# Optimization experiments

Measured on AMD Instinct MI355X. Metric: run time of the kernel, lower is better.

## Reference

```python
import jax, jax.numpy as jnp
import numpy as np

TAU = 0.05


def setup_inputs() -> dict:
    key = jax.random.key(0)
    ks = jax.random.split(key, 4)
    N, D, F, E = 8192, 1024, 4096, 8
    h = jax.random.normal(ks[0], (N, D), dtype=jnp.float32)
    Wr = jax.random.normal(ks[1], (D, E), dtype=jnp.float32) * (1.0 / np.sqrt(D))
    br = jnp.zeros((E,), dtype=jnp.float32)
    W1 = jax.random.normal(ks[2], (E, D, F), dtype=jnp.float32) * (1.0 / np.sqrt(D))
    b1 = jnp.zeros((E, F), dtype=jnp.float32)
    W2 = jax.random.normal(ks[3], (E, F, D), dtype=jnp.float32) * (1.0 / np.sqrt(F))
    b2 = jnp.zeros((E, D), dtype=jnp.float32)
    return {"h": h, "Wr": Wr, "br": br, "W1": W1, "b1": b1, "W2": W2, "b2": b2}


def reference(h, Wr, br, W1, b1, W2, b2):
    # Router: linear + softmax over experts -> [N, E]
    weights = jax.nn.softmax(h @ Wr + br, axis=-1)
    # Threshold mask (weights > tau); masked_weights = weights * mask
    masked_w = jnp.where(weights > TAU, weights, 0.0)  # [N, E]
    # Experts: 2-layer MLP per expert, computed batched over the expert axis.
    # hid: [N, E, F]
    hid = jax.nn.gelu(jnp.einsum('nd,edf->nef', h, W1) + b1)
    # expert outputs: [N, E, D]
    out_e = jnp.einsum('nef,efd->ned', hid, W2) + b2
    # Weighted combine; zero masked weights annihilate inactive experts,
    # matching the conditional sum (and the zeros_like fallback when none active).
    return jnp.einsum('ne,ned->nd', masked_w, out_e)
```

## Files before the change

### kernel.cpp

```cpp
#include <hip/hip_runtime.h>
#include <hip/hip_bf16.h>
#include <cstdint>
#include <cstddef>

typedef __attribute__((ext_vector_type(8))) __bf16 bf16x8;
typedef __attribute__((ext_vector_type(4))) float f32x4;
typedef __attribute__((ext_vector_type(4))) unsigned short us4;

#define GLOAD_LDS16(g, l)                                                        \
    __builtin_amdgcn_global_load_lds(                                            \
        (const __attribute__((address_space(1))) void*)(g),                      \
        (__attribute__((address_space(3))) void*)(l), 16, 0, 0)

static __device__ __forceinline__ unsigned short f2bf(float x) {
    unsigned int u = __builtin_bit_cast(unsigned int, x);
    return (unsigned short)((u + 0x7FFFu + ((u >> 16) & 1u)) >> 16);
}

static __device__ __forceinline__ float gelu_fast(float x) {
    const float p = x * x;
    const float u = x * fmaf(0.0713548162726f, p, 1.59576912161f);
    const float t = __expf(-u);
    return x * __builtin_amdgcn_rcpf(1.0f + t);
}

__global__ __launch_bounds__(256) void moe_router_kernel(
    const float* __restrict__ h, const float* __restrict__ Wr,
    const float* __restrict__ br, unsigned short* __restrict__ hbf,
    float* __restrict__ mw)
{
    const int lane = threadIdx.x & 63, wave = threadIdx.x >> 6;
    const int n = blockIdx.x * 4 + wave;
    const float* hr = h + (size_t)n * 1024;
    const int base = lane * 16;

    float xs[16];
#pragma unroll
    for (int q = 0; q < 4; ++q) {
        f32x4 v = *(const f32x4*)(hr + base + q * 4);
        xs[q * 4 + 0] = v[0]; xs[q * 4 + 1] = v[1];
        xs[q * 4 + 2] = v[2]; xs[q * 4 + 3] = v[3];
    }
    float acc[8] = {0.f, 0.f, 0.f, 0.f, 0.f, 0.f, 0.f, 0.f};
#pragma unroll
    for (int j = 0; j < 16; ++j) {
        const float x = xs[j];
        const f32x4 w0 = *(const f32x4*)(Wr + (size_t)(base + j) * 8);
        const f32x4 w1 = *(const f32x4*)(Wr + (size_t)(base + j) * 8 + 4);
        acc[0] += x * w0[0]; acc[1] += x * w0[1]; acc[2] += x * w0[2]; acc[3] += x * w0[3];
        acc[4] += x * w1[0]; acc[5] += x * w1[1]; acc[6] += x * w1[2]; acc[7] += x * w1[3];
    }
#pragma unroll
    for (int q = 0; q < 4; ++q) {
        us4 o;
        o[0] = f2bf(xs[q * 4 + 0]); o[1] = f2bf(xs[q * 4 + 1]);
        o[2] = f2bf(xs[q * 4 + 2]); o[3] = f2bf(xs[q * 4 + 3]);
        *(us4*)(hbf + (size_t)n * 1024 + base + q * 4) = o;
    }
#pragma unroll
    for (int m = 32; m >= 1; m >>= 1)
#pragma unroll
        for (int e = 0; e < 8; ++e) acc[e] += __shfl_xor(acc[e], m, 64);

    if (lane == 0) {
        float l[8]; float mx = -1e30f;
#pragma unroll
        for (int e = 0; e < 8; ++e) { l[e] = acc[e] + br[e]; mx = fmaxf(mx, l[e]); }
        float s = 0.f;
#pragma unroll
        for (int e = 0; e < 8; ++e) { l[e] = __expf(l[e] - mx); s += l[e]; }
        const float inv = 1.0f / s;
#pragma unroll
        for (int e = 0; e < 8; ++e) {
            const float w = l[e] * inv;
            mw[(size_t)n * 8 + e] = (w > 0.05f) ? w : 0.0f;
        }
    }
}

__global__ __launch_bounds__(256) void moe_tcvt_kernel(
    const float* __restrict__ in, unsigned short* __restrict__ out,
    int ls, size_t in_es, int os, size_t out_es)
{
    __shared__ unsigned short t[32][33];
    const int e = blockIdx.z;
    const int r = threadIdx.x >> 3, c = (threadIdx.x & 7) * 4;
    const float* I = in + (size_t)e * in_es + (size_t)(blockIdx.x * 32 + r) * ls + blockIdx.y * 32 + c;
    f32x4 v = *(const f32x4*)I;
    t[r][c + 0] = f2bf(v[0]); t[r][c + 1] = f2bf(v[1]);
    t[r][c + 2] = f2bf(v[2]); t[r][c + 3] = f2bf(v[3]);
    __syncthreads();
    unsigned short* O = out + (size_t)e * out_es + (size_t)(blockIdx.y * 32 + r) * os + blockIdx.x * 32 + c;
    us4 o;
    o[0] = t[c + 0][r]; o[1] = t[c + 1][r]; o[2] = t[c + 2][r]; o[3] = t[c + 3][r];
    *(us4*)O = o;
}

#define MFMA_QUAD(MB, NB, AF, BQ)                                              \
  _Pragma("unroll") for (int mi_ = 0; mi_ < 4; ++mi_)                          \
  _Pragma("unroll") for (int ni_ = 0; ni_ < 2; ++ni_) {                        \
      acc[(MB)+mi_][(NB)+ni_] = __builtin_amdgcn_mfma_f32_16x16x32_bf16(       \
          BQ[ni_][1], AF[mi_][1], __builtin_amdgcn_mfma_f32_16x16x32_bf16(     \
          BQ[ni_][0], AF[mi_][0], acc[(MB)+mi_][(NB)+ni_], 0, 0, 0), 0, 0, 0); \
  }

#define BARX()   __builtin_amdgcn_s_barrier()
#define SBX()    __builtin_amdgcn_sched_barrier(0)
#define LGKM(N)  asm volatile("s_waitcnt lgkmcnt(" #N ")" ::: "memory")
#define VMC(N)   asm volatile("s_waitcnt vmcnt(" #N ")" ::: "memory")
#define PRIO1()  __builtin_amdgcn_s_setprio(1)
#define PRIO0()  __builtin_amdgcn_s_setprio(0)

template <int MODE>
__global__ __launch_bounds__(512) void moe_gemm8p(
    const unsigned short* __restrict__ A, int ldga,
    const unsigned short* __restrict__ Bbase, size_t estride, int ldb,
    const float* __restrict__ b1, const float* __restrict__ mw,
    unsigned short* __restrict__ Cg, int ldc,
    float* __restrict__ part,
    int logFc, int f0glob, int kspan, int init)
{
    __shared__ unsigned short sh[65536];
    char* sm = (char*)sh;
    const int XA = 0, XB = 32768, YA = 65536, YB = 98304;

    const int tid = threadIdx.x, lane = tid & 63, wv = tid >> 6;
    const int wr = wv >> 2, wc = wv & 3;

    int bx, by;
    if constexpr (MODE == 0) {
        const int orig = blockIdx.x + blockIdx.y * 32;
        const int c8 = orig & 7, j = orig >> 3;
        bx = c8 * 4 + (j & 3); by = j >> 2;
    } else {
        const int orig = blockIdx.x + blockIdx.y * 32;
        const int c8 = orig & 7, j = orig >> 3;
        bx = c8 * 4 + (j >> 2); by = j & 3;
    }
    const int m0 = bx * 256;
    const int n0 = by * 256;

    const int z = (MODE == 1) ? blockIdx.z : 0;
    const int klo = z * kspan;
    float* Cacc = (MODE == 1) ? part + (size_t)z * (8192 * 1024) : nullptr;

    int e0 = 0, fb = 0;
    const unsigned short* gB0 = nullptr;
    const int rl0 = tid >> 3;
    const int gs8 = ((tid & 7) ^ (rl0 & 7)) * 8;
    if constexpr (MODE == 0) {
        e0 = n0 >> logFc; fb = n0 - (e0 << logFc);
        gB0 = Bbase + (size_t)e0 * estride + (size_t)(fb + rl0) * ldb + gs8;
    }
    const unsigned short* gA0 = A + (size_t)(m0 + rl0) * ldga + gs8;
    const int dstw = wv * 1024;

    auto stageA = [&](int reg, int kk, int q) {
        GLOAD_LDS16(gA0 + kk + (size_t)(q * 64) * ldga,
                    sm + reg + (q >> 1) * 16384 + (q & 1) * 8192 + dstw);
    };
    auto stageB = [&](int reg, int kk, int q) {
        const unsigned short* gb;
        if constexpr (MODE == 0) {
            gb = gB0 + kk;
        } else {
            const int e = kk >> logFc, kc = kk - (e << logFc);
            gb = Bbase + (size_t)e * estride + (size_t)(n0 + rl0) * ldb + kc + gs8;
        }
        GLOAD_LDS16(gb + (size_t)(q * 64) * ldb,
                    sm + reg + (q >> 1) * 16384 + (q & 1) * 8192 + dstw);
    };

    const int l15 = lane & 15, l4 = lane >> 4, l7 = lane & 7;
    const int sA0 = (wr * 128 + l15) * 128 + (((0 + l4) ^ l7) << 4);
    const int sA1 = (wr * 128 + l15) * 128 + (((4 + l4) ^ l7) << 4);
    const int sB0 = (wc * 64 + l15) * 128 + (((0 + l4) ^ l7) << 4);
    const int sB1 = (wc * 64 + l15) * 128 + (((4 + l4) ^ l7) << 4);

    f32x4 acc[8][4] = {};
    bf16x8 afL[4][2], afH[4][2], bqL[2][2], bqH[2][2];

#define RD_AFL(BASE) _Pragma("unroll") for (int mi_=0;mi_<4;++mi_){            \
      afL[mi_][0] = *(const bf16x8*)(sm + (BASE) + sA0 + mi_*2048);            \
      afL[mi_][1] = *(const bf16x8*)(sm + (BASE) + sA1 + mi_*2048); }
#define RD_AFH(BASE) _Pragma("unroll") for (int mi_=0;mi_<4;++mi_){            \
      afH[mi_][0] = *(const bf16x8*)(sm + (BASE) + sA0 + (4+mi_)*2048);        \
      afH[mi_][1] = *(const bf16x8*)(sm + (BASE) + sA1 + (4+mi_)*2048); }
#define RD_BQL(BASE) _Pragma("unroll") for (int ni_=0;ni_<2;++ni_){            \
      bqL[ni_][0] = *(const bf16x8*)(sm + (BASE) + sB0 + ni_*2048);            \
      bqL[ni_][1] = *(const bf16x8*)(sm + (BASE) + sB1 + ni_*2048); }
#define RD_BQH(BASE) _Pragma("unroll") for (int ni_=0;ni_<2;++ni_){            \
      bqH[ni_][0] = *(const bf16x8*)(sm + (BASE) + sB0 + (2+ni_)*2048);        \
      bqH[ni_][1] = *(const bf16x8*)(sm + (BASE) + sB1 + (2+ni_)*2048); }

    const int niter = kspan >> 7;

#pragma unroll
    for (int q = 0; q < 4; ++q) { stageA(XA, klo, q); stageB(XB, klo, q); }
#pragma unroll
    for (int q = 0; q < 4; ++q) { stageA(YA, klo + 64, q); stageB(YB, klo + 64, q); }
    VMC(8); SBX();
    BARX();
    RD_AFL(XA); RD_BQL(XB);

    for (int it = 0; it < niter; ++it) {
        const int kX2 = klo + it * 128 + 128;
        const int kY2 = klo + it * 128 + 192;
        const bool g = (it + 1 < niter);
        RD_BQH(XB);
        BARX(); LGKM(4); SBX(); PRIO1(); MFMA_QUAD(0, 0, afL, bqL); PRIO0(); BARX();
        RD_AFH(XA);
        if (g) { stageA(XA, kX2, 0); stageA(XA, kX2, 2); }
        BARX(); LGKM(8); SBX(); PRIO1(); MFMA_QUAD(0, 2, afL, bqH); PRIO0(); BARX();
        if (g) { stageB(XB, kX2, 0); stageB(XB, kX2, 1); }
        BARX(); LGKM(0); SBX(); PRIO1(); MFMA_QUAD(4, 0, afH, bqL); PRIO0(); BARX();
        if (g) { stageA(XA, kX2, 1); stageA(XA, kX2, 3);
                 stageB(XB, kX2, 2); stageB(XB, kX2, 3);
                 VMC(8); } else { VMC(0); }
        SBX();
        BARX();
        RD_AFL(YA); RD_BQL(YB);
        SBX(); PRIO1(); MFMA_QUAD(4, 2, afH, bqH); PRIO0(); BARX();
        RD_BQH(YB);
        BARX(); LGKM(4); SBX(); PRIO1(); MFMA_QUAD(0, 0, afL, bqL); PRIO0(); BARX();
        RD_AFH(YA);
        if (g) { stageA(YA, kY2, 0); stageA(YA, kY2, 2); }
        BARX(); LGKM(8); SBX(); PRIO1(); MFMA_QUAD(0, 2, afL, bqH); PRIO0(); BARX();
        if (g) { stageB(YB, kY2, 0); stageB(YB, kY2, 1); }
        BARX(); LGKM(0); SBX(); PRIO1(); MFMA_QUAD(4, 0, afH, bqL); PRIO0(); BARX();
        if (g) { stageA(YA, kY2, 1); stageA(YA, kY2, 3);
                 stageB(YB, kY2, 2); stageB(YB, kY2, 3);
                 VMC(8); } else { VMC(0); }
        SBX();
        BARX();
        if (g) { RD_AFL(XA); RD_BQL(XB); }
        SBX(); PRIO1(); MFMA_QUAD(4, 2, afH, bqH); PRIO0(); BARX();
    }

    const int nr0v = l4 * 4;
    if constexpr (MODE == 0) {
        const float* b1p = b1 + (size_t)e0 * 4096 + f0glob + fb;
        f32x4 b1v[4];
#pragma unroll
        for (int j = 0; j < 4; ++j)
            b1v[j] = *(const f32x4*)(b1p + wc * 64 + j * 16 + nr0v);
#pragma unroll
        for (int i = 0; i < 8; ++i) {
            const int token = m0 + wr * 128 + i * 16 + l15;
            const float w = mw[(size_t)token * 8 + e0];
            unsigned short* crow = Cg + (size_t)token * ldc + n0;
#pragma unroll
            for (int j = 0; j < 4; ++j) {
                const int n = wc * 64 + j * 16 + nr0v;
                us4 o;
#pragma unroll
                for (int r = 0; r < 4; ++r)
                    o[r] = f2bf(w * gelu_fast(acc[i][j][r] + b1v[j][r]));
                *(us4*)(crow + n) = o;
            }
        }
    } else {
#pragma unroll
        for (int i = 0; i < 8; ++i) {
            const int row = m0 + wr * 128 + i * 16 + l15;
            float* cp = Cacc + (size_t)row * 1024 + n0;
#pragma unroll
            for (int j = 0; j < 4; ++j) {
                const int n = wc * 64 + j * 16 + nr0v;
                if (init) {
                    *(f32x4*)(cp + n) = acc[i][j];
                } else {
                    f32x4 old = *(const f32x4*)(cp + n);
                    *(f32x4*)(cp + n) = old + acc[i][j];
                }
            }
        }
    }
}

__global__ __launch_bounds__(256) void moe_combine_kernel(
    const float* __restrict__ part, int S,
    float* __restrict__ out, const float* __restrict__ mw,
    const float* __restrict__ b2)
{
    const int n = blockIdx.x, t = threadIdx.x;
    const int d = t * 4;
    f32x4 v = *(const f32x4*)(part + (size_t)n * 1024 + d);
    for (int z = 1; z < S; ++z)
        v = v + *(const f32x4*)(part + (size_t)z * (8192 * 1024) + (size_t)n * 1024 + d);
#pragma unroll
    for (int e = 0; e < 8; ++e) {
        const float w = mw[(size_t)n * 8 + e];
        const f32x4 b = *(const f32x4*)(b2 + (size_t)e * 1024 + d);
        v = v + w * b;
    }
    *(f32x4*)(out + (size_t)n * 1024 + d) = v;
}

extern "C" void kernel_launch(void* const* d_in, const int* in_sizes, int n_in,
                              void* d_out, int out_size, void* d_ws, size_t ws_size,
                              hipStream_t stream)
{
    (void)in_sizes; (void)n_in; (void)out_size;
    const float* h  = (const float*)d_in[0];
    const float* Wr = (const float*)d_in[1];
    const float* br = (const float*)d_in[2];
    const float* W1 = (const float*)d_in[3];
    const float* b1 = (const float*)d_in[4];
    const float* W2 = (const float*)d_in[5];
    const float* b2 = (const float*)d_in[6];
    float* out = (float*)d_out;

    const int N = 8192, D = 1024, F = 4096, E = 8;
    const int S = 2;
    auto al = [](size_t x) { return (x + 255) & ~(size_t)255; };
    const size_t sz_hbf = al((size_t)N * D * 2);
    const size_t sz_mw  = al((size_t)N * E * 4);
    const size_t sz_pt1 = al((size_t)N * D * 4);
    auto tot = [&](int fc) {
        size_t s = sz_hbf + sz_mw + al((size_t)N * ((size_t)E * fc + 32) * 2);
        s += al((size_t)E * fc * D * 2) * 2;
        s += (size_t)S * sz_pt1;
        return s;
    };
    int Fc;
    if      (tot(1024) <= ws_size) Fc = 1024;
    else if (tot(512)  <= ws_size) Fc = 512;
    else                           Fc = 256;
    const int logFc = (Fc == 1024) ? 10 : (Fc == 512) ? 9 : 8;
    const int Kc = E * Fc;
    const int ldAp = Kc + 32;

    char* p = (char*)d_ws;
    unsigned short* hbf = (unsigned short*)p; p += sz_hbf;
    float* mwp  = (float*)p; p += sz_mw;
    unsigned short* ghid = (unsigned short*)p; p += al((size_t)N * (size_t)ldAp * 2);
    unsigned short* W1t  = (unsigned short*)p; p += al((size_t)E * Fc * D * 2);
    unsigned short* W2t  = (unsigned short*)p; p += al((size_t)E * Fc * D * 2);
    float* part = (float*)p;

    moe_router_kernel<<<N / 4, 256, 0, stream>>>(h, Wr, br, hbf, mwp);

    const int nch = F / Fc;
    for (int c = 0; c < nch; ++c) {
        moe_tcvt_kernel<<<dim3(D / 32, Fc / 32, E), 256, 0, stream>>>(
            W1 + (size_t)c * Fc, W1t, F, (size_t)D * F, D, (size_t)Fc * D);
        moe_tcvt_kernel<<<dim3(Fc / 32, D / 32, E), 256, 0, stream>>>(
            W2 + (size_t)c * Fc * D, W2t, D, (size_t)F * D, Fc, (size_t)D * Fc);

        moe_gemm8p<0><<<dim3(32, Kc / 256, 1), 512, 0, stream>>>(
            hbf, 1024, W1t, (size_t)Fc * D, 1024, b1, mwp, ghid, ldAp, nullptr,
            logFc, c * Fc, 1024, 0);

        moe_gemm8p<1><<<dim3(32, 4, S), 512, 0, stream>>>(
            ghid, ldAp, W2t, (size_t)D * Fc, Fc, nullptr, nullptr, nullptr, 0, part,
            logFc, 0, Kc / S, (c == 0) ? 1 : 0);
    }

    moe_combine_kernel<<<N, 256, 0, stream>>>(part, S, out, mwp, b2);
}
```

Baseline: 1.243 ms.

## Gather active tokens per expert to skip inactive rows in first GEMM

Adds a compaction kernel that builds a per-expert list of tokens whose routing weight passes the threshold, and makes the first expert GEMM gather A rows through that list and exit early for tiles past the active count. Inactive (token, expert) hidden slices are zero-filled once up front so the second GEMM stays dense and still correct. It also raises the preferred F chunk size so fewer chunk iterations are launched. The cost is extra kernels, a memset and an atomic, gathered global loads for A, and a larger workspace requirement.

```diff
diff --git a/kernel.cpp b/kernel.cpp
--- a/kernel.cpp
+++ b/kernel.cpp
@@ -74,6 +74,48 @@
         for (int e = 0; e < 8; ++e) {
             const float w = l[e] * inv;
             mw[(size_t)n * 8 + e] = (w > 0.05f) ? w : 0.0f;
+        }
+    }
+}
+
+__global__ __launch_bounds__(256) void moe_compact_kernel(
+    const float* __restrict__ mw, int* __restrict__ cnt, int* __restrict__ toklist)
+{
+    const int n = blockIdx.x * 256 + threadIdx.x;
+    const int lane = threadIdx.x & 63;
+#pragma unroll
+    for (int e = 0; e < 8; ++e) {
+        const bool act = mw[(size_t)n * 8 + e] > 0.f;
+        const unsigned long long mask = __ballot(act);
+        const int cw = __popcll(mask);
+        if (cw) {
+            int base = 0;
+            const int leader = __ffsll((unsigned long long)mask) - 1;
+            if (lane == leader) base = atomicAdd(&cnt[e], cw);
+            base = __shfl(base, leader);
+            if (act) {
+                const int pre = __popcll(mask & ((1ull << lane) - 1ull));
+                toklist[e * 8192 + base + pre] = n;
+            }
+        }
+    }
+}
+
+__global__ __launch_bounds__(256) void moe_zfill_kernel(
+    const float* __restrict__ mw, unsigned short* __restrict__ ghid,
+    int Fc, int ldAp)
+{
+    const int n = blockIdx.x, t = threadIdx.x;
+    __shared__ float w[8];
+    if (t < 8) w[t] = mw[(size_t)n * 8 + t];
+    __syncthreads();
+    const us4 z = {0, 0, 0, 0};
+#pragma unroll
+    for (int e = 0; e < 8; ++e) {
+        if (w[e] == 0.f) {
+            unsigned short* row = ghid + (size_t)n * ldAp + e * Fc;
+            for (int c = t * 4; c < Fc; c += 1024)
+                *(us4*)(row + c) = z;
         }
     }
 }
@@ -118,6 +160,7 @@
     const float* __restrict__ b1, const float* __restrict__ mw,
     unsigned short* __restrict__ Cg, int ldc,
     float* __restrict__ part,
+    const int* __restrict__ cnt, const int* __restrict__ toklist,
     int logFc, int f0glob, int kspan, int init)
 {
     __shared__ unsigned short sh[65536];
@@ -148,16 +191,39 @@
     const unsigned short* gB0 = nullptr;
     const int rl0 = tid >> 3;
     const int gs8 = ((tid & 7) ^ (rl0 & 7)) * 8;
+    const int l15 = lane & 15, l4 = lane >> 4, l7 = lane & 7;
+
+    int Me = 0;
+    int idxS[4], idxE[8];
     if constexpr (MODE == 0) {
         e0 = n0 >> logFc; fb = n0 - (e0 << logFc);
         gB0 = Bbase + (size_t)e0 * estride + (size_t)(fb + rl0) * ldb + gs8;
+        Me = cnt[e0];
+        if (m0 >= Me) return;
+        const int* tl = toklist + e0 * 8192;
+#pragma unroll
+        for (int q = 0; q < 4; ++q) {
+            int pos = m0 + rl0 + q * 64; if (pos > Me - 1) pos = Me - 1;
+            idxS[q] = tl[pos];
+        }
+#pragma unroll
+        for (int i = 0; i < 8; ++i) {
+            int pos = m0 + wr * 128 + i * 16 + l15; if (pos > Me - 1) pos = Me - 1;
+            idxE[i] = tl[pos];
+        }
+        VMC(0); SBX();
     }
     const unsigned short* gA0 = A + (size_t)(m0 + rl0) * ldga + gs8;
     const int dstw = wv * 1024;
 
     auto stageA = [&](int reg, int kk, int q) {
-        GLOAD_LDS16(gA0 + kk + (size_t)(q * 64) * ldga,
-                    sm + reg + (q >> 1) * 16384 + (q & 1) * 8192 + dstw);
+        const unsigned short* ga;
+        if constexpr (MODE == 0) {
+            ga = A + (size_t)idxS[q] * ldga + gs8 + kk;
+        } else {
+            ga = gA0 + kk + (size_t)(q * 64) * ldga;
+        }
+        GLOAD_LDS16(ga, sm + reg + (q >> 1) * 16384 + (q & 1) * 8192 + dstw);
     };
     auto stageB = [&](int reg, int kk, int q) {
         const unsigned short* gb;
@@ -171,7 +237,6 @@
                     sm + reg + (q >> 1) * 16384 + (q & 1) * 8192 + dstw);
     };
 
-    const int l15 = lane & 15, l4 = lane >> 4, l7 = lane & 7;
     const int sA0 = (wr * 128 + l15) * 128 + (((0 + l4) ^ l7) << 4);
     const int sA1 = (wr * 128 + l15) * 128 + (((4 + l4) ^ l7) << 4);
     const int sB0 = (wc * 64 + l15) * 128 + (((0 + l4) ^ l7) << 4);
@@ -246,17 +311,20 @@
             b1v[j] = *(const f32x4*)(b1p + wc * 64 + j * 16 + nr0v);
 #pragma unroll
         for (int i = 0; i < 8; ++i) {
-            const int token = m0 + wr * 128 + i * 16 + l15;
-            const float w = mw[(size_t)token * 8 + e0];
-            unsigned short* crow = Cg + (size_t)token * ldc + n0;
-#pragma unroll
-            for (int j = 0; j < 4; ++j) {
-                const int n = wc * 64 + j * 16 + nr0v;
-                us4 o;
-#pragma unroll
-                for (int r = 0; r < 4; ++r)
-                    o[r] = f2bf(w * gelu_fast(acc[i][j][r] + b1v[j][r]));
-                *(us4*)(crow + n) = o;
+            const int pos = m0 + wr * 128 + i * 16 + l15;
+            if (pos < Me) {
+                const int token = idxE[i];
+                const float w = mw[(size_t)token * 8 + e0];
+                unsigned short* crow = Cg + (size_t)token * ldc + n0;
+#pragma unroll
+                for (int j = 0; j < 4; ++j) {
+                    const int n = wc * 64 + j * 16 + nr0v;
+                    us4 o;
+#pragma unroll
+                    for (int r = 0; r < 4; ++r)
+                        o[r] = f2bf(w * gelu_fast(acc[i][j][r] + b1v[j][r]));
+                    *(us4*)(crow + n) = o;
+                }
             }
         }
     } else {
@@ -316,30 +384,38 @@
     auto al = [](size_t x) { return (x + 255) & ~(size_t)255; };
     const size_t sz_hbf = al((size_t)N * D * 2);
     const size_t sz_mw  = al((size_t)N * E * 4);
+    const size_t sz_cnt = al(8 * 4);
+    const size_t sz_tok = al((size_t)N * E * 4);
     const size_t sz_pt1 = al((size_t)N * D * 4);
     auto tot = [&](int fc) {
-        size_t s = sz_hbf + sz_mw + al((size_t)N * ((size_t)E * fc + 32) * 2);
-        s += al((size_t)E * fc * D * 2) * 2;
-        s += (size_t)S * sz_pt1;
+        size_t s = sz_hbf + sz_mw + sz_cnt + sz_tok
+                 + al((size_t)N * ((size_t)E * fc + 32) * 2)
+                 + al((size_t)E * fc * D * 2) * 2
+                 + (size_t)S * sz_pt1;
         return s;
     };
     int Fc;
-    if      (tot(1024) <= ws_size) Fc = 1024;
-    else if (tot(512)  <= ws_size) Fc = 512;
-    else                           Fc = 256;
-    const int logFc = (Fc == 1024) ? 10 : (Fc == 512) ? 9 : 8;
+    if      (tot(2048) <= ws_size) Fc = 2048;
+    else if (tot(1024) <= ws_size) Fc = 1024;
+    else                           Fc = 512;
+    const int logFc = (Fc == 2048) ? 11 : (Fc == 1024) ? 10 : 9;
     const int Kc = E * Fc;
     const int ldAp = Kc + 32;
 
     char* p = (char*)d_ws;
     unsigned short* hbf = (unsigned short*)p; p += sz_hbf;
     float* mwp  = (float*)p; p += sz_mw;
+    int*   cnt  = (int*)p;   p += sz_cnt;
+    int*   tok  = (int*)p;   p += sz_tok;
     unsigned short* ghid = (unsigned short*)p; p += al((size_t)N * (size_t)ldAp * 2);
     unsigned short* W1t  = (unsigned short*)p; p += al((size_t)E * Fc * D * 2);
     unsigned short* W2t  = (unsigned short*)p; p += al((size_t)E * Fc * D * 2);
     float* part = (float*)p;
 
     moe_router_kernel<<<N / 4, 256, 0, stream>>>(h, Wr, br, hbf, mwp);
+    hipMemsetAsync(cnt, 0, 8 * sizeof(int), stream);
+    moe_compact_kernel<<<N / 256, 256, 0, stream>>>(mwp, cnt, tok);
+    moe_zfill_kernel<<<N, 256, 0, stream>>>(mwp, ghid, Fc, ldAp);
 
     const int nch = F / Fc;
     for (int c = 0; c < nch; ++c) {
@@ -350,11 +426,11 @@
 
         moe_gemm8p<0><<<dim3(32, Kc / 256, 1), 512, 0, stream>>>(
             hbf, 1024, W1t, (size_t)Fc * D, 1024, b1, mwp, ghid, ldAp, nullptr,
-            logFc, c * Fc, 1024, 0);
+            cnt, tok, logFc, c * Fc, 1024, 0);
 
         moe_gemm8p<1><<<dim3(32, 4, S), 512, 0, stream>>>(
             ghid, ldAp, W2t, (size_t)D * Fc, Fc, nullptr, nullptr, nullptr, 0, part,
-            logFc, 0, Kc / S, (c == 0) ? 1 : 0);
+            nullptr, nullptr, logFc, 0, Kc / S, (c == 0) ? 1 : 0);
     }
 
     moe_combine_kernel<<<N, 256, 0, stream>>>(part, S, out, mwp, b2);
```

Measured after the change: 1.258 ms. About the same (+1.2%).
